# Kernel optimization log

Hardware: AMD Instinct MI355X
Metric: run time of the kernel (lower is better)

The kernel has to match this reference:

```python
import jax, jax.numpy as jnp
import numpy as np

TAU = 2.0
V_TH = 1.0


def setup_inputs() -> dict:
    key = jax.random.key(0)
    k1, k2, k3 = jax.random.split(key, 3)
    T, B, H = 128, 64, 1024
    x = jax.random.normal(k1, (T, B, H), dtype=jnp.float32)
    # nn.Linear(H, H, bias=False) weights, shape [out, in]
    W1 = jax.random.normal(k2, (H, H), dtype=jnp.float32) / np.sqrt(H)
    W2 = jax.random.normal(k3, (H, H), dtype=jnp.float32) / np.sqrt(H)
    return {"x": x, "W1": W1, "W2": W2}


def _lif_scan(x_proj):
    # x_proj: [T, B, H]; membrane v starts at 0.
    def step(v, xt):
        h = v + (xt - v) / TAU          # leaky integrate
        s = (h >= V_TH).astype(h.dtype)  # hard-threshold spike
        v_new = h * (1.0 - s)            # soft reset (to 0 on spike)
        return v_new, s

    v0 = jnp.zeros(x_proj.shape[1:], dtype=x_proj.dtype)
    _, spikes = jax.lax.scan(step, v0, x_proj)
    return spikes  # [T, B, H]


def reference(x, W1, W2):
    # fc1 applied per timestep == one batched GEMM over [T*B, H]
    x_proj = jnp.einsum('tbh,oh->tbo', x, W1)
    spike = _lif_scan(x_proj)
    out = jnp.einsum('tbh,oh->tbo', spike, W2)
    return out
```

## Files before the change

kernel.cpp:

```cpp
#include <hip/hip_runtime.h>
#include <hip/hip_bf16.h>
#include <stdint.h>

#define TT 128
#define BB 64
#define HH 1024
#define MM (TT * BB)
#define NLANE (BB * HH)
#define DELTA 3.0e-5
#define CAPL 32768
#define LO_SCALE 4096.0f
#define F16_ONE 0x3C00

typedef __attribute__((ext_vector_type(8))) _Float16 f16x8;
typedef __attribute__((ext_vector_type(4))) float f32x4;

#define GLOAD16(g, l)                                                        \
    __builtin_amdgcn_global_load_lds(                                        \
        (const __attribute__((address_space(1))) unsigned int*)(g),          \
        (__attribute__((address_space(3))) unsigned int*)(l), 16, 0, 0)

static __device__ __forceinline__ unsigned short f16_bits(float f) {
    _Float16 h = (_Float16)f;
    return *reinterpret_cast<unsigned short*>(&h);
}

__global__ __launch_bounds__(256) void split2_kernel(const float* __restrict__ src,
                                                     unsigned short* __restrict__ hi,
                                                     unsigned short* __restrict__ lo,
                                                     int n4) {
    const int i = blockIdx.x * 256 + threadIdx.x;
    if (i >= n4) return;
    float4 x = reinterpret_cast<const float4*>(src)[i];
    float v[4] = {x.x, x.y, x.z, x.w};
    unsigned short hb[4], lb[4];
#pragma unroll
    for (int c = 0; c < 4; c++) {
        _Float16 hh = (_Float16)v[c];
        hb[c] = *reinterpret_cast<unsigned short*>(&hh);
        lb[c] = f16_bits((v[c] - (float)hh) * LO_SCALE);
    }
    reinterpret_cast<ushort4*>(hi)[i] = make_ushort4(hb[0], hb[1], hb[2], hb[3]);
    reinterpret_cast<ushort4*>(lo)[i] = make_ushort4(lb[0], lb[1], lb[2], lb[3]);
}

__global__ __launch_bounds__(256) void cast_f16(const float* __restrict__ src,
                                                unsigned short* __restrict__ dst,
                                                int n) {
    const int i = blockIdx.x * 256 + threadIdx.x;
    if (i < n) dst[i] = f16_bits(src[i]);
}

__global__ __launch_bounds__(256) void gemm1_mfma(const unsigned short* __restrict__ Ah,
                                                  const unsigned short* __restrict__ Al,
                                                  const unsigned short* __restrict__ Bh,
                                                  const unsigned short* __restrict__ Bl,
                                                  float* __restrict__ C) {
    __shared__ short AsH[128 * 32];
    __shared__ short AsL[128 * 32];
    __shared__ short BsH[128 * 32];
    __shared__ short BsL[128 * 32];

    const int tid = threadIdx.x;
    const int lane = tid & 63;
    const int wave = tid >> 6;
    const int m0 = blockIdx.x * 128;
    const int n0 = blockIdx.y * 128;
    const int wm = (wave >> 1) * 64;
    const int wn = (wave & 1) * 64;

    const int rsel = lane & 15;
    const int part = lane >> 4;

    int adrA[4], adrB[4];
#pragma unroll
    for (int i = 0; i < 4; i++) {
        const int ra = wm + i * 16 + rsel;
        const int rb = wn + i * 16 + rsel;
        adrA[i] = ra * 32 + (part ^ ((ra >> 1) & 3)) * 8;
        adrB[i] = rb * 32 + (part ^ ((rb >> 1) & 3)) * 8;
    }

    f32x4 acc1[4][4] = {};
    f32x4 acc2[4][4] = {};

    for (int k0 = 0; k0 < HH; k0 += 32) {
#pragma unroll
        for (int p = 0; p < 2; p++) {
            const int c = tid + p * 256;
            const int cb = wave * 64 + p * 256;
            const int row = c >> 2;
            const int pslot = c & 3;
            const int pdata = pslot ^ ((row >> 1) & 3);
            const size_t goA = (size_t)(m0 + row) * HH + k0 + pdata * 8;
            const size_t goB = (size_t)(n0 + row) * HH + k0 + pdata * 8;
            GLOAD16(&Ah[goA], &AsH[cb * 8]);
            GLOAD16(&Al[goA], &AsL[cb * 8]);
            GLOAD16(&Bh[goB], &BsH[cb * 8]);
            GLOAD16(&Bl[goB], &BsL[cb * 8]);
        }
        __syncthreads();

        f16x8 aH[4], aL[4], bH[4], bL[4];
#pragma unroll
        for (int mi = 0; mi < 4; mi++) {
            aH[mi] = *reinterpret_cast<f16x8*>(&AsH[adrA[mi]]);
            aL[mi] = *reinterpret_cast<f16x8*>(&AsL[adrA[mi]]);
        }
#pragma unroll
        for (int ni = 0; ni < 4; ni++) {
            bH[ni] = *reinterpret_cast<f16x8*>(&BsH[adrB[ni]]);
            bL[ni] = *reinterpret_cast<f16x8*>(&BsL[adrB[ni]]);
        }

#pragma unroll
        for (int mi = 0; mi < 4; mi++)
#pragma unroll
            for (int ni = 0; ni < 4; ni++) {
                acc1[mi][ni] = __builtin_amdgcn_mfma_f32_16x16x32_f16(aH[mi], bH[ni], acc1[mi][ni], 0, 0, 0);
                acc2[mi][ni] = __builtin_amdgcn_mfma_f32_16x16x32_f16(aH[mi], bL[ni], acc2[mi][ni], 0, 0, 0);
                acc2[mi][ni] = __builtin_amdgcn_mfma_f32_16x16x32_f16(aL[mi], bH[ni], acc2[mi][ni], 0, 0, 0);
            }

        __syncthreads();
    }

    const int col = lane & 15;
    const int quad = lane >> 4;
    const float inv = 1.0f / LO_SCALE;
#pragma unroll
    for (int mi = 0; mi < 4; mi++)
#pragma unroll
        for (int ni = 0; ni < 4; ni++) {
            const int m = m0 + wm + mi * 16 + quad * 4;
            const int n = n0 + wn + ni * 16 + col;
            float* dst = &C[(size_t)m * HH + n];
#pragma unroll
            for (int r = 0; r < 4; r++)
                dst[(size_t)r * HH] = fmaf(acc2[mi][ni][r], inv, acc1[mi][ni][r]);
        }
}

__global__ __launch_bounds__(256) void lif_scan_flag(const float* __restrict__ xp,
                                                     unsigned short* __restrict__ sp,
                                                     int* __restrict__ count,
                                                     int* __restrict__ list) {
    const int idx = blockIdx.x * 256 + threadIdx.x;
    double v = 0.0;
    bool flg = false;
#pragma unroll 4
    for (int t = 0; t < TT; t++) {
        const double x = (double)xp[(size_t)t * NLANE + idx];
        const double h = v + (x - v) * 0.5;
        const bool s = (h >= 1.0);
        flg |= (fabs(h - 1.0) < DELTA);
        v = s ? 0.0 : h;
        sp[(size_t)t * NLANE + idx] = s ? (unsigned short)F16_ONE : (unsigned short)0;
    }
    if (flg) {
        const int i = atomicAdd(count, 1);
        list[i] = idx;
    }
}

__global__ __launch_bounds__(256) void recompute_dots(const float* __restrict__ X,
                                                      const float* __restrict__ W1,
                                                      const int* __restrict__ count,
                                                      const int* __restrict__ list,
                                                      double* __restrict__ hraw) {
    const int cnt = *count;
    const int lim = (cnt < CAPL ? cnt : CAPL);
    const long ntask = (long)lim * TT;
    const int ln = threadIdx.x & 63;
    const long wid = (long)blockIdx.x * 4 + (threadIdx.x >> 6);
    const long nwaves = (long)gridDim.x * 4;

    for (long task = wid; task < ntask; task += nwaves) {
        const int li = (int)(task >> 7);
        const int t = (int)(task & (TT - 1));
        const int lane = list[li];
        const int b = lane >> 10;
        const int h = lane & (HH - 1);
        const float4* x4 = reinterpret_cast<const float4*>(X + (size_t)(t * BB + b) * HH);
        const float4* w4 = reinterpret_cast<const float4*>(W1 + (size_t)h * HH);

        double s0 = 0.0, s1 = 0.0, s2 = 0.0, s3 = 0.0;
#pragma unroll
        for (int i = 0; i < 4; i++) {
            const float4 xa = x4[ln + i * 64];
            const float4 wa = w4[ln + i * 64];
            s0 = fma((double)xa.x, (double)wa.x, s0);
            s1 = fma((double)xa.y, (double)wa.y, s1);
            s2 = fma((double)xa.z, (double)wa.z, s2);
            s3 = fma((double)xa.w, (double)wa.w, s3);
        }
        double s = (s0 + s1) + (s2 + s3);
#pragma unroll
        for (int off = 32; off >= 1; off >>= 1)
            s += __shfl_down(s, off);
        if (ln == 0) hraw[task] = s;
    }
}

__global__ __launch_bounds__(256) void rescan_lanes(const float* __restrict__ X,
                                                    const float* __restrict__ W1,
                                                    const int* __restrict__ count,
                                                    const int* __restrict__ list,
                                                    const double* __restrict__ hraw,
                                                    unsigned short* __restrict__ sp) {
    const int li = blockIdx.x * 256 + threadIdx.x;
    const int cnt = *count;
    if (li >= cnt) return;
    const int lane = list[li];

    double v = 0.0;
    if (li < CAPL) {
        const double* hb = hraw + (size_t)li * TT;
        for (int t = 0; t < TT; t++) {
            const double h = v + (hb[t] - v) * 0.5;
            const bool s = (h >= 1.0);
            v = s ? 0.0 : h;
            sp[(size_t)t * NLANE + lane] = s ? (unsigned short)F16_ONE : (unsigned short)0;
        }
    } else {
        const int b = lane >> 10;
        const int h = lane & (HH - 1);
        const float* wrow = W1 + (size_t)h * HH;
        for (int t = 0; t < TT; t++) {
            const float* xrow = X + (size_t)(t * BB + b) * HH;
            double d = 0.0;
            for (int k = 0; k < HH; k++)
                d = fma((double)xrow[k], (double)wrow[k], d);
            const double hh = v + (d - v) * 0.5;
            const bool s = (hh >= 1.0);
            v = s ? 0.0 : hh;
            sp[(size_t)t * NLANE + lane] = s ? (unsigned short)F16_ONE : (unsigned short)0;
        }
    }
}

__global__ __launch_bounds__(256) void gemm2_mfma(const unsigned short* __restrict__ S,
                                                  const unsigned short* __restrict__ W,
                                                  float* __restrict__ O) {
    __shared__ short As[128 * 32];
    __shared__ short Bs[128 * 32];

    const int tid = threadIdx.x;
    const int lane = tid & 63;
    const int wave = tid >> 6;
    const int m0 = blockIdx.x * 128;
    const int n0 = blockIdx.y * 128;
    const int wm = (wave >> 1) * 64;
    const int wn = (wave & 1) * 64;

    const int rsel = lane & 15;
    const int part = lane >> 4;

    int adrA[4], adrB[4];
#pragma unroll
    for (int i = 0; i < 4; i++) {
        const int ra = wm + i * 16 + rsel;
        const int rb = wn + i * 16 + rsel;
        adrA[i] = ra * 32 + (part ^ ((ra >> 1) & 3)) * 8;
        adrB[i] = rb * 32 + (part ^ ((rb >> 1) & 3)) * 8;
    }

    f32x4 acc[4][4] = {};

    for (int k0 = 0; k0 < HH; k0 += 32) {
#pragma unroll
        for (int p = 0; p < 2; p++) {
            const int c = tid + p * 256;
            const int cb = wave * 64 + p * 256;
            const int row = c >> 2;
            const int pslot = c & 3;
            const int pdata = pslot ^ ((row >> 1) & 3);
            GLOAD16(&S[(size_t)(m0 + row) * HH + k0 + pdata * 8], &As[cb * 8]);
            GLOAD16(&W[(size_t)(n0 + row) * HH + k0 + pdata * 8], &Bs[cb * 8]);
        }
        __syncthreads();

        f16x8 a[4], b[4];
#pragma unroll
        for (int mi = 0; mi < 4; mi++)
            a[mi] = *reinterpret_cast<f16x8*>(&As[adrA[mi]]);
#pragma unroll
        for (int ni = 0; ni < 4; ni++)
            b[ni] = *reinterpret_cast<f16x8*>(&Bs[adrB[ni]]);

#pragma unroll
        for (int mi = 0; mi < 4; mi++)
#pragma unroll
            for (int ni = 0; ni < 4; ni++)
                acc[mi][ni] = __builtin_amdgcn_mfma_f32_16x16x32_f16(
                    a[mi], b[ni], acc[mi][ni], 0, 0, 0);

        __syncthreads();
    }

    const int col = lane & 15;
    const int quad = lane >> 4;
#pragma unroll
    for (int mi = 0; mi < 4; mi++)
#pragma unroll
        for (int ni = 0; ni < 4; ni++) {
            const int m = m0 + wm + mi * 16 + quad * 4;
            const int n = n0 + wn + ni * 16 + col;
            float* dst = &O[(size_t)m * HH + n];
#pragma unroll
            for (int r = 0; r < 4; r++)
                dst[(size_t)r * HH] = acc[mi][ni][r];
        }
}

extern "C" void kernel_launch(void* const* d_in, const int* in_sizes, int n_in,
                              void* d_out, int out_size, void* d_ws, size_t ws_size,
                              hipStream_t stream) {
    const float* x  = (const float*)d_in[0];
    const float* W1 = (const float*)d_in[1];
    const float* W2 = (const float*)d_in[2];
    float* out = (float*)d_out;

    char* ws = (char*)d_ws;
    const size_t szX = (size_t)MM * HH;
    const size_t szW = (size_t)HH * HH;

    unsigned short* Xhi  = (unsigned short*)ws;
    unsigned short* Xlo  = Xhi + szX;
    unsigned short* W1hi = Xlo + szX;
    unsigned short* W1lo = W1hi + szW;
    unsigned short* w2h  = W1lo + szW;
    int*            list = (int*)(w2h + szW);
    int*            cnt  = list + NLANE;
    float*          xp   = (float*)(((uintptr_t)(cnt + 64) + 255) & ~(uintptr_t)255);
    unsigned short* sp   = Xhi;
    double*         hraw = (double*)xp;

    hipMemsetAsync(cnt, 0, sizeof(int), stream);

    split2_kernel<<<(int)(szX / 4 / 256), 256, 0, stream>>>(x, Xhi, Xlo, (int)(szX / 4));
    split2_kernel<<<(int)(szW / 4 / 256), 256, 0, stream>>>(W1, W1hi, W1lo, (int)(szW / 4));
    cast_f16<<<(int)((szW + 255) / 256), 256, 0, stream>>>(W2, w2h, (int)szW);

    dim3 g1(MM / 128, HH / 128);
    gemm1_mfma<<<g1, 256, 0, stream>>>(Xhi, Xlo, W1hi, W1lo, xp);

    lif_scan_flag<<<NLANE / 256, 256, 0, stream>>>(xp, sp, cnt, list);

    recompute_dots<<<2048, 256, 0, stream>>>(x, W1, cnt, list, hraw);
    rescan_lanes<<<NLANE / 256, 256, 0, stream>>>(x, W1, cnt, list, hraw, sp);

    dim3 g2(MM / 128, HH / 128);
    gemm2_mfma<<<g2, 256, 0, stream>>>(sp, w2h, out);
}
```

Before: 258.5 us.

## Fuse prep kernels, switch GEMM1 split to bf16, deepen GEMM2 K tile, prefetch scan

Merges the two split kernels, the W2 cast and the counter memset into one launch. GEMM1 now splits into bf16 hi/lo parts and uses a single accumulator with bf16 MFMA, which drops the second accumulator set and the rescale. The flag tolerance is widened to cover the coarser bf16 split. GEMM2 doubles its K tile to 64 with a new XOR swizzle to halve barrier count, and the LIF scan keeps a 4-deep register prefetch ring; the wider tolerance may send more lanes to the slow fp64 recompute path.

```diff
diff --git a/kernel.cpp b/kernel.cpp
--- a/kernel.cpp
+++ b/kernel.cpp
@@ -7,11 +7,11 @@
 #define HH 1024
 #define MM (TT * BB)
 #define NLANE (BB * HH)
-#define DELTA 3.0e-5
+#define DELTA 1.0e-4
 #define CAPL 32768
-#define LO_SCALE 4096.0f
 #define F16_ONE 0x3C00
 
+typedef __attribute__((ext_vector_type(8))) short bf16x8;
 typedef __attribute__((ext_vector_type(8))) _Float16 f16x8;
 typedef __attribute__((ext_vector_type(4))) float f32x4;
 
@@ -20,35 +20,58 @@
         (const __attribute__((address_space(1))) unsigned int*)(g),          \
         (__attribute__((address_space(3))) unsigned int*)(l), 16, 0, 0)
 
+static __device__ __forceinline__ unsigned short bf16_bits(float f) {
+    __hip_bfloat16 b = __float2bfloat16(f);
+    return *reinterpret_cast<unsigned short*>(&b);
+}
 static __device__ __forceinline__ unsigned short f16_bits(float f) {
     _Float16 h = (_Float16)f;
     return *reinterpret_cast<unsigned short*>(&h);
 }
 
-__global__ __launch_bounds__(256) void split2_kernel(const float* __restrict__ src,
-                                                     unsigned short* __restrict__ hi,
-                                                     unsigned short* __restrict__ lo,
-                                                     int n4) {
-    const int i = blockIdx.x * 256 + threadIdx.x;
-    if (i >= n4) return;
-    float4 x = reinterpret_cast<const float4*>(src)[i];
-    float v[4] = {x.x, x.y, x.z, x.w};
+__global__ __launch_bounds__(256) void prep_fused(const float* __restrict__ x,
+                                                  const float* __restrict__ W1,
+                                                  const float* __restrict__ W2,
+                                                  unsigned short* __restrict__ Xhi,
+                                                  unsigned short* __restrict__ Xlo,
+                                                  unsigned short* __restrict__ W1hi,
+                                                  unsigned short* __restrict__ W1lo,
+                                                  unsigned short* __restrict__ w2h,
+                                                  int* __restrict__ cnt) {
+    const int bid = blockIdx.x;
+    if (bid == 0 && threadIdx.x == 0) *cnt = 0;
+
+    const float* src;
+    unsigned short *hi, *lo;
+    int i;
+    bool split;
+    if (bid < 8192) {
+        i = bid * 256 + threadIdx.x;
+        src = x; hi = Xhi; lo = Xlo; split = true;
+    } else if (bid < 9216) {
+        i = (bid - 8192) * 256 + threadIdx.x;
+        src = W1; hi = W1hi; lo = W1lo; split = true;
+    } else {
+        i = (bid - 9216) * 256 + threadIdx.x;
+        src = W2; hi = w2h; lo = nullptr; split = false;
+    }
+
+    float4 v4 = reinterpret_cast<const float4*>(src)[i];
+    float v[4] = {v4.x, v4.y, v4.z, v4.w};
     unsigned short hb[4], lb[4];
 #pragma unroll
     for (int c = 0; c < 4; c++) {
-        _Float16 hh = (_Float16)v[c];
-        hb[c] = *reinterpret_cast<unsigned short*>(&hh);
-        lb[c] = f16_bits((v[c] - (float)hh) * LO_SCALE);
+        if (split) {
+            hb[c] = bf16_bits(v[c]);
+            __hip_bfloat16 hh = *reinterpret_cast<__hip_bfloat16*>(&hb[c]);
+            lb[c] = bf16_bits(v[c] - __bfloat162float(hh));
+        } else {
+            hb[c] = f16_bits(v[c]);
+        }
     }
     reinterpret_cast<ushort4*>(hi)[i] = make_ushort4(hb[0], hb[1], hb[2], hb[3]);
-    reinterpret_cast<ushort4*>(lo)[i] = make_ushort4(lb[0], lb[1], lb[2], lb[3]);
-}
-
-__global__ __launch_bounds__(256) void cast_f16(const float* __restrict__ src,
-                                                unsigned short* __restrict__ dst,
-                                                int n) {
-    const int i = blockIdx.x * 256 + threadIdx.x;
-    if (i < n) dst[i] = f16_bits(src[i]);
+    if (split)
+        reinterpret_cast<ushort4*>(lo)[i] = make_ushort4(lb[0], lb[1], lb[2], lb[3]);
 }
 
 __global__ __launch_bounds__(256) void gemm1_mfma(const unsigned short* __restrict__ Ah,
@@ -81,8 +104,7 @@
         adrB[i] = rb * 32 + (part ^ ((rb >> 1) & 3)) * 8;
     }
 
-    f32x4 acc1[4][4] = {};
-    f32x4 acc2[4][4] = {};
+    f32x4 acc[4][4] = {};
 
     for (int k0 = 0; k0 < HH; k0 += 32) {
 #pragma unroll
@@ -101,25 +123,25 @@
         }
         __syncthreads();
 
-        f16x8 aH[4], aL[4], bH[4], bL[4];
+        bf16x8 aH[4], aL[4], bH[4], bL[4];
 #pragma unroll
         for (int mi = 0; mi < 4; mi++) {
-            aH[mi] = *reinterpret_cast<f16x8*>(&AsH[adrA[mi]]);
-            aL[mi] = *reinterpret_cast<f16x8*>(&AsL[adrA[mi]]);
+            aH[mi] = *reinterpret_cast<bf16x8*>(&AsH[adrA[mi]]);
+            aL[mi] = *reinterpret_cast<bf16x8*>(&AsL[adrA[mi]]);
         }
 #pragma unroll
         for (int ni = 0; ni < 4; ni++) {
-            bH[ni] = *reinterpret_cast<f16x8*>(&BsH[adrB[ni]]);
-            bL[ni] = *reinterpret_cast<f16x8*>(&BsL[adrB[ni]]);
+            bH[ni] = *reinterpret_cast<bf16x8*>(&BsH[adrB[ni]]);
+            bL[ni] = *reinterpret_cast<bf16x8*>(&BsL[adrB[ni]]);
         }
 
 #pragma unroll
         for (int mi = 0; mi < 4; mi++)
 #pragma unroll
             for (int ni = 0; ni < 4; ni++) {
-                acc1[mi][ni] = __builtin_amdgcn_mfma_f32_16x16x32_f16(aH[mi], bH[ni], acc1[mi][ni], 0, 0, 0);
-                acc2[mi][ni] = __builtin_amdgcn_mfma_f32_16x16x32_f16(aH[mi], bL[ni], acc2[mi][ni], 0, 0, 0);
-                acc2[mi][ni] = __builtin_amdgcn_mfma_f32_16x16x32_f16(aL[mi], bH[ni], acc2[mi][ni], 0, 0, 0);
+                acc[mi][ni] = __builtin_amdgcn_mfma_f32_16x16x32_bf16(aH[mi], bH[ni], acc[mi][ni], 0, 0, 0);
+                acc[mi][ni] = __builtin_amdgcn_mfma_f32_16x16x32_bf16(aH[mi], bL[ni], acc[mi][ni], 0, 0, 0);
+                acc[mi][ni] = __builtin_amdgcn_mfma_f32_16x16x32_bf16(aL[mi], bH[ni], acc[mi][ni], 0, 0, 0);
             }
 
         __syncthreads();
@@ -127,7 +149,6 @@
 
     const int col = lane & 15;
     const int quad = lane >> 4;
-    const float inv = 1.0f / LO_SCALE;
 #pragma unroll
     for (int mi = 0; mi < 4; mi++)
 #pragma unroll
@@ -137,7 +158,7 @@
             float* dst = &C[(size_t)m * HH + n];
 #pragma unroll
             for (int r = 0; r < 4; r++)
-                dst[(size_t)r * HH] = fmaf(acc2[mi][ni][r], inv, acc1[mi][ni][r]);
+                dst[(size_t)r * HH] = acc[mi][ni][r];
         }
 }
 
@@ -146,11 +167,18 @@
                                                      int* __restrict__ count,
                                                      int* __restrict__ list) {
     const int idx = blockIdx.x * 256 + threadIdx.x;
+    const float* p = xp + idx;
+    float buf[4];
+#pragma unroll
+    for (int i = 0; i < 4; i++) buf[i] = p[(size_t)i * NLANE];
+
     double v = 0.0;
     bool flg = false;
 #pragma unroll 4
     for (int t = 0; t < TT; t++) {
-        const double x = (double)xp[(size_t)t * NLANE + idx];
+        const float xf = buf[t & 3];
+        if (t + 4 < TT) buf[t & 3] = p[(size_t)(t + 4) * NLANE];
+        const double x = (double)xf;
         const double h = v + (x - v) * 0.5;
         const bool s = (h >= 1.0);
         flg |= (fabs(h - 1.0) < DELTA);
@@ -242,8 +270,8 @@
 __global__ __launch_bounds__(256) void gemm2_mfma(const unsigned short* __restrict__ S,
                                                   const unsigned short* __restrict__ W,
                                                   float* __restrict__ O) {
-    __shared__ short As[128 * 32];
-    __shared__ short Bs[128 * 32];
+    __shared__ short As[128 * 64];
+    __shared__ short Bs[128 * 64];
 
     const int tid = threadIdx.x;
     const int lane = tid & 63;
@@ -254,46 +282,53 @@
     const int wn = (wave & 1) * 64;
 
     const int rsel = lane & 15;
-    const int part = lane >> 4;
-
-    int adrA[4], adrB[4];
+    const int qpart = lane >> 4;
+
+    int adrA[4][2], adrB[4][2];
 #pragma unroll
     for (int i = 0; i < 4; i++) {
         const int ra = wm + i * 16 + rsel;
         const int rb = wn + i * 16 + rsel;
-        adrA[i] = ra * 32 + (part ^ ((ra >> 1) & 3)) * 8;
-        adrB[i] = rb * 32 + (part ^ ((rb >> 1) & 3)) * 8;
+#pragma unroll
+        for (int h = 0; h < 2; h++) {
+            const int pa = h * 4 + qpart;
+            adrA[i][h] = ra * 64 + ((pa ^ (ra & 7)) * 8);
+            adrB[i][h] = rb * 64 + ((pa ^ (rb & 7)) * 8);
+        }
     }
 
     f32x4 acc[4][4] = {};
 
-    for (int k0 = 0; k0 < HH; k0 += 32) {
-#pragma unroll
-        for (int p = 0; p < 2; p++) {
+    for (int k0 = 0; k0 < HH; k0 += 64) {
+#pragma unroll
+        for (int p = 0; p < 4; p++) {
             const int c = tid + p * 256;
             const int cb = wave * 64 + p * 256;
-            const int row = c >> 2;
-            const int pslot = c & 3;
-            const int pdata = pslot ^ ((row >> 1) & 3);
+            const int row = c >> 3;
+            const int pslot = c & 7;
+            const int pdata = pslot ^ (row & 7);
             GLOAD16(&S[(size_t)(m0 + row) * HH + k0 + pdata * 8], &As[cb * 8]);
             GLOAD16(&W[(size_t)(n0 + row) * HH + k0 + pdata * 8], &Bs[cb * 8]);
         }
         __syncthreads();
 
-        f16x8 a[4], b[4];
-#pragma unroll
-        for (int mi = 0; mi < 4; mi++)
-            a[mi] = *reinterpret_cast<f16x8*>(&As[adrA[mi]]);
-#pragma unroll
-        for (int ni = 0; ni < 4; ni++)
-            b[ni] = *reinterpret_cast<f16x8*>(&Bs[adrB[ni]]);
-
-#pragma unroll
-        for (int mi = 0; mi < 4; mi++)
+#pragma unroll
+        for (int h = 0; h < 2; h++) {
+            f16x8 a[4], b[4];
+#pragma unroll
+            for (int mi = 0; mi < 4; mi++)
+                a[mi] = *reinterpret_cast<f16x8*>(&As[adrA[mi][h]]);
 #pragma unroll
             for (int ni = 0; ni < 4; ni++)
-                acc[mi][ni] = __builtin_amdgcn_mfma_f32_16x16x32_f16(
-                    a[mi], b[ni], acc[mi][ni], 0, 0, 0);
+                b[ni] = *reinterpret_cast<f16x8*>(&Bs[adrB[ni][h]]);
+
+#pragma unroll
+            for (int mi = 0; mi < 4; mi++)
+#pragma unroll
+                for (int ni = 0; ni < 4; ni++)
+                    acc[mi][ni] = __builtin_amdgcn_mfma_f32_16x16x32_f16(
+                        a[mi], b[ni], acc[mi][ni], 0, 0, 0);
+        }
 
         __syncthreads();
     }
@@ -336,11 +371,7 @@
     unsigned short* sp   = Xhi;
     double*         hraw = (double*)xp;
 
-    hipMemsetAsync(cnt, 0, sizeof(int), stream);
-
-    split2_kernel<<<(int)(szX / 4 / 256), 256, 0, stream>>>(x, Xhi, Xlo, (int)(szX / 4));
-    split2_kernel<<<(int)(szW / 4 / 256), 256, 0, stream>>>(W1, W1hi, W1lo, (int)(szW / 4));
-    cast_f16<<<(int)((szW + 255) / 256), 256, 0, stream>>>(W2, w2h, (int)szW);
+    prep_fused<<<10240, 256, 0, stream>>>(x, W1, W2, Xhi, Xlo, W1hi, W1lo, w2h, cnt);
 
     dim3 g1(MM / 128, HH / 128);
     gemm1_mfma<<<g1, 256, 0, stream>>>(Xhi, Xlo, W1hi, W1lo, xp);
```

Measured after the change: 248.7 us. -3.8%, faster.
